# Performance work log

Measured on AMD Instinct MI355X. Metric: run time of the kernel, lower is better.

## Reference

```python
import jax, jax.numpy as jnp
import numpy as np

TEMPERATURE = 1.0
PRED_PER_IM = 100
INVALID = np.arange(60, 80)  # invalid class logit indices (constant)


def setup_inputs() -> dict:
    key = jax.random.key(0)
    k1, k2, k3, k4, k5 = jax.random.split(key, 5)
    B, Q, C = 256, 1000, 81
    return {
        "pred_logits": jax.random.normal(k1, (B, Q, C), jnp.float32),
        "pred_obj": jax.random.normal(k2, (B, Q), jnp.float32),
        "pred_boxes": jax.random.uniform(k3, (B, Q, 4), jnp.float32),  # cxcywh in [0,1)
        "pred_unk": jax.random.normal(k4, (B, Q), jnp.float32),
        "target_sizes": jax.random.uniform(k5, (B, 2), jnp.float32, minval=480.0, maxval=1333.0),  # (h, w)
    }


def _postprocess(pred_logits, pred_obj, pred_boxes, pred_unk, target_sizes):
    B, Q, C = pred_logits.shape
    # mask invalid classes with a huge negative logit
    logits = pred_logits.at[:, :, INVALID].set(-1e11)
    obj_prob = jnp.exp(-TEMPERATURE * pred_obj)[..., None]            # [B,Q,1]
    prob = obj_prob * jax.nn.sigmoid(logits)                          # [B,Q,C]
    prob = prob.at[:, :, INVALID].set(0.0)
    unk = jax.nn.sigmoid(pred_unk)                                    # [B,Q]
    prob = prob * (1.0 - unk[..., None])
    prob = prob.at[:, :, -1].set(obj_prob[..., 0] * unk)              # unknown class slot
    # flattened top-k over (query, class)
    scores, idx = jax.lax.top_k(prob.reshape(B, Q * C), PRED_PER_IM)  # [B,K]
    topk_boxes = idx // C
    labels = idx % C
    # cxcywh -> xyxy
    cx, cy, w, h = jnp.split(pred_boxes, 4, axis=-1)
    xyxy = jnp.concatenate([cx - 0.5 * w, cy - 0.5 * h, cx + 0.5 * w, cy + 0.5 * h], axis=-1)
    boxes = jnp.take_along_axis(xyxy, topk_boxes[..., None], axis=1)  # [B,K,4]
    img_h, img_w = target_sizes[:, 0], target_sizes[:, 1]
    scale = jnp.stack([img_w, img_h, img_w, img_h], axis=1)           # [B,4]
    boxes = boxes * scale[:, None, :]
    return scores, labels, boxes


def reference(pred_logits, pred_obj, pred_boxes, pred_unk, target_sizes):
    return _postprocess(pred_logits, pred_obj, pred_boxes, pred_unk, target_sizes)
```

## Files before the change

### kernel.cpp

```cpp
#include <hip/hip_runtime.h>
#include <math.h>

#define BATCH  256
#define NQ     1000
#define NC     81
#define QC     81000
#define CHUNKS (QC / 4)
#define TOPK   100
#define NBINS  4096
#define CAP    2048
#define NT     1024

__device__ __forceinline__ float sigmoidf(float x) {
    if (x >= 0.f) return 1.f / (1.f + expf(-x));
    float e = expf(x);
    return e / (1.f + e);
}

__device__ __forceinline__ float fast_sig(float x) {
    return __builtin_amdgcn_rcpf(1.f + __expf(-x));
}

struct Smem {
    float    P[NQ];
    float    Pm2[NQ];
    float    op[NQ];
    float    omun[NQ];
    float    last[NQ];
    unsigned hist[NBINS];
    uint2    cand[CAP];
    unsigned cnt;
    unsigned thr;
};

__device__ unsigned scan_threshold(Smem& s, int tid) {
    __syncthreads();
    if (tid < 64) {
        unsigned c = 0;
        #pragma unroll
        for (int j = 0; j < 64; j += 4) {
            uint4 h = *(const uint4*)&s.hist[tid * 64 + j];
            c += h.x + h.y + h.z + h.w;
        }
        unsigned ssum = c;
        #pragma unroll
        for (int off = 1; off < 64; off <<= 1) {
            unsigned o = __shfl_down(ssum, off, 64);
            if (tid + off < 64) ssum += o;
        }
        unsigned long long bal = __ballot(ssum >= TOPK);
        int cb = 63 - __clzll(bal);
        unsigned tb = 0;
        if (cb >= 0) {
            unsigned S_cb = __shfl(ssum, cb, 64);
            unsigned c_cb = __shfl(c, cb, 64);
            unsigned acc  = S_cb - c_cb;
            unsigned fs = s.hist[cb * 64 + tid];
            #pragma unroll
            for (int off = 1; off < 64; off <<= 1) {
                unsigned o = __shfl_down(fs, off, 64);
                if (tid + off < 64) fs += o;
            }
            unsigned long long bal2 = __ballot(acc + fs >= TOPK);
            int fb = 63 - __clzll(bal2);
            tb = (unsigned)(cb * 64 + fb);
        }
        if (tid == 0) s.thr = tb;
    }
    __syncthreads();
    return s.thr;
}

__device__ __forceinline__ void chunk_hist(Smem& s, const float4& v4, int q, int c,
                                           unsigned thbits) {
    float xs[4] = {v4.x, v4.y, v4.z, v4.w};
    #pragma unroll
    for (int k = 0; k < 4; ++k) {
        int ck = c + k, qk = q;
        if (ck >= NC) { ck -= NC; ++qk; }
        if (ck < 60) {
            unsigned u = __float_as_uint(s.P[qk] * fast_sig(xs[k]));
            if (u >= thbits) atomicAdd(&s.hist[u >> 19], 1u);
        }
    }
}

__device__ __forceinline__ void chunk_collect(Smem& s, const float4& v4, int q, int c,
                                              unsigned thbits) {
    float xs[4] = {v4.x, v4.y, v4.z, v4.w};
    #pragma unroll
    for (int k = 0; k < 4; ++k) {
        int ck = c + k, qk = q;
        if (ck >= NC) { ck -= NC; ++qk; }
        if (ck < 60) {
            unsigned u = __float_as_uint(s.P[qk] * fast_sig(xs[k]));
            if (u >= thbits) {
                float pv = (s.op[qk] * sigmoidf(xs[k])) * s.omun[qk];
                unsigned p = atomicAdd(&s.cnt, 1u);
                if (p < CAP)
                    s.cand[p] = make_uint2(__float_as_uint(pv), (unsigned)(qk * NC + ck));
            }
        }
    }
}

template <bool COLLECT>
__device__ void scan(Smem& s, const float4* __restrict__ lg4, unsigned thbits, int tid) {
    int q = (4 * tid) / NC;
    int c = 4 * tid - q * NC;
    for (int base = tid; base < CHUNKS; base += 4 * NT) {
        float4 vv[4]; bool dd[4]; int qs[4], cs[4];
        int qq = q, cc = c;
        #pragma unroll
        for (int t = 0; t < 4; ++t) {
            int i4 = base + t * NT;
            qs[t] = qq; cs[t] = cc;
            dd[t] = (i4 < CHUNKS) && (__float_as_uint(s.Pm2[qq]) >= thbits);
            if (dd[t]) vv[t] = lg4[i4];
            cc += 46; qq += 50; if (cc >= NC) { cc -= NC; ++qq; }
        }
        #pragma unroll
        for (int t = 0; t < 4; ++t) if (dd[t]) {
            if (COLLECT) chunk_collect(s, vv[t], qs[t], cs[t], thbits);
            else         chunk_hist   (s, vv[t], qs[t], cs[t], thbits);
        }
        c += 22; q += 202; if (c >= NC) { c -= NC; ++q; }
    }
}

__device__ void collect80(Smem& s, unsigned thbits, int tid) {
    for (int q = tid; q < NQ; q += NT) {
        unsigned u = __float_as_uint(s.last[q]);
        if (u >= thbits) {
            unsigned p = atomicAdd(&s.cnt, 1u);
            if (p < CAP) s.cand[p] = make_uint2(u, (unsigned)(q * NC + 80));
        }
    }
}

__global__ __launch_bounds__(NT) void postprocess_kernel(
    const float* __restrict__ logits,
    const float* __restrict__ obj,
    const float* __restrict__ boxes,
    const float* __restrict__ unk,
    const float* __restrict__ tsz,
    float* __restrict__ out)
{
    __shared__ Smem s;
    const int b   = blockIdx.x;
    const int tid = threadIdx.x;
    const float4* lg4 = (const float4*)(logits + (size_t)b * QC);

    {
        int i = tid * 4;
        *(uint4*)&s.hist[i] = make_uint4(0u, 0u, 0u, 0u);
    }
    if (tid == 0) s.cnt = 0;
    for (int q = tid; q < NQ; q += NT) {
        float op = expf(-obj[b * NQ + q]);
        float un = sigmoidf(unk[b * NQ + q]);
        float om = 1.f - un;
        s.op[q] = op; s.omun[q] = om; s.P[q] = op * om; s.last[q] = op * un;
    }
    __syncthreads();

    for (int q = tid; q < NQ; q += NT) {
        float pm = s.P[q];
        if (q + 1 < NQ) pm = fmaxf(pm, s.P[q + 1]);
        s.Pm2[q] = pm;
        atomicAdd(&s.hist[__float_as_uint(s.last[q]) >> 19], 1u);
    }

    unsigned t0 = scan_threshold(s, tid);

    scan<false>(s, lg4, t0 << 19, tid);

    unsigned tF = scan_threshold(s, tid);

    unsigned thC = ((tF >= 1) ? tF - 1 : 0) << 19;
    scan<true>(s, lg4, thC, tid);
    collect80(s, thC, tid);
    __syncthreads();

    if (s.cnt > CAP) {
        __syncthreads();
        if (tid == 0) s.cnt = 0;
        __syncthreads();
        scan<true>(s, lg4, tF << 19, tid);
        collect80(s, tF << 19, tid);
        __syncthreads();
    }

    const int m = (int)min(s.cnt, (unsigned)CAP);

    const float* bx = boxes + (size_t)b * NQ * 4;
    const float img_h = tsz[b * 2 + 0];
    const float img_w = tsz[b * 2 + 1];
    float* o_sc = out + (size_t)b * TOPK;
    float* o_lb = out + (size_t)BATCH * TOPK + (size_t)b * TOPK;
    float* o_bx = out + (size_t)2 * BATCH * TOPK + (size_t)b * TOPK * 4;

    for (int i = tid; i < m; i += NT) {
        uint2 ci = s.cand[i];
        int r = 0;
        for (int j = 0; j < m; ++j) {
            uint2 cj = s.cand[j];
            r += (cj.x > ci.x) || (cj.x == ci.x && cj.y < ci.y);
        }
        if (r < TOPK) {
            int ei = (int)ci.y;
            o_sc[r] = __uint_as_float(ci.x);
            o_lb[r] = (float)(ei % NC);
            int q = ei / NC;
            float cx = bx[q * 4 + 0];
            float cy = bx[q * 4 + 1];
            float w  = bx[q * 4 + 2];
            float h  = bx[q * 4 + 3];
            o_bx[r * 4 + 0] = (cx - 0.5f * w) * img_w;
            o_bx[r * 4 + 1] = (cy - 0.5f * h) * img_h;
            o_bx[r * 4 + 2] = (cx + 0.5f * w) * img_w;
            o_bx[r * 4 + 3] = (cy + 0.5f * h) * img_h;
        }
    }
}

extern "C" void kernel_launch(void* const* d_in, const int* in_sizes, int n_in,
                              void* d_out, int out_size, void* d_ws, size_t ws_size,
                              hipStream_t stream) {
    const float* pred_logits = (const float*)d_in[0];
    const float* pred_obj    = (const float*)d_in[1];
    const float* pred_boxes  = (const float*)d_in[2];
    const float* pred_unk    = (const float*)d_in[3];
    const float* target_sz   = (const float*)d_in[4];
    float* out = (float*)d_out;
    postprocess_kernel<<<BATCH, NT, 0, stream>>>(
        pred_logits, pred_obj, pred_boxes, pred_unk, target_sz, out);
}
```

Before: 145.3 us.

## Compact surviving query rows and scan only their logit chunks

Before each histogram or collect pass, a shared-memory list is built of the query rows whose max-probability bound reaches the threshold. Work is then spread evenly across only those rows' float4 chunks, instead of striding over every chunk and skipping dead ones by predicate. The intent is to remove idle loop iterations and load imbalance across threads when few rows survive. The cost is extra barriers, an atomic-based compaction step, and an integer divide by 21 per work item.

```diff
diff --git a/kernel.cpp b/kernel.cpp
--- a/kernel.cpp
+++ b/kernel.cpp
@@ -29,6 +29,8 @@
     float    last[NQ];
     unsigned hist[NBINS];
     uint2    cand[CAP];
+    int      rowlist[NQ];
+    unsigned nrows;
     unsigned cnt;
     unsigned thr;
 };
@@ -71,7 +73,8 @@
     return s.thr;
 }
 
-__device__ __forceinline__ void chunk_hist(Smem& s, const float4& v4, int q, int c,
+template <bool COLLECT>
+__device__ __forceinline__ void proc_chunk(Smem& s, const float4& v4, int q, int c,
                                            unsigned thbits) {
     float xs[4] = {v4.x, v4.y, v4.z, v4.w};
     #pragma unroll
@@ -80,51 +83,45 @@
         if (ck >= NC) { ck -= NC; ++qk; }
         if (ck < 60) {
             unsigned u = __float_as_uint(s.P[qk] * fast_sig(xs[k]));
-            if (u >= thbits) atomicAdd(&s.hist[u >> 19], 1u);
-        }
-    }
-}
-
-__device__ __forceinline__ void chunk_collect(Smem& s, const float4& v4, int q, int c,
-                                              unsigned thbits) {
-    float xs[4] = {v4.x, v4.y, v4.z, v4.w};
-    #pragma unroll
-    for (int k = 0; k < 4; ++k) {
-        int ck = c + k, qk = q;
-        if (ck >= NC) { ck -= NC; ++qk; }
-        if (ck < 60) {
-            unsigned u = __float_as_uint(s.P[qk] * fast_sig(xs[k]));
             if (u >= thbits) {
-                float pv = (s.op[qk] * sigmoidf(xs[k])) * s.omun[qk];
-                unsigned p = atomicAdd(&s.cnt, 1u);
-                if (p < CAP)
-                    s.cand[p] = make_uint2(__float_as_uint(pv), (unsigned)(qk * NC + ck));
+                if (!COLLECT) {
+                    atomicAdd(&s.hist[u >> 19], 1u);
+                } else {
+                    float pv = (s.op[qk] * sigmoidf(xs[k])) * s.omun[qk];
+                    unsigned p = atomicAdd(&s.cnt, 1u);
+                    if (p < CAP)
+                        s.cand[p] = make_uint2(__float_as_uint(pv),
+                                               (unsigned)(qk * NC + ck));
+                }
             }
         }
     }
 }
 
+__device__ void build_rows(Smem& s, unsigned thbits, int tid) {
+    __syncthreads();
+    if (tid == 0) s.nrows = 0;
+    __syncthreads();
+    for (int q = tid; q < NQ; q += NT)
+        if (__float_as_uint(s.Pm2[q]) >= thbits)
+            s.rowlist[atomicAdd(&s.nrows, 1u)] = q;
+    __syncthreads();
+}
+
 template <bool COLLECT>
-__device__ void scan(Smem& s, const float4* __restrict__ lg4, unsigned thbits, int tid) {
-    int q = (4 * tid) / NC;
-    int c = 4 * tid - q * NC;
-    for (int base = tid; base < CHUNKS; base += 4 * NT) {
-        float4 vv[4]; bool dd[4]; int qs[4], cs[4];
-        int qq = q, cc = c;
-        #pragma unroll
-        for (int t = 0; t < 4; ++t) {
-            int i4 = base + t * NT;
-            qs[t] = qq; cs[t] = cc;
-            dd[t] = (i4 < CHUNKS) && (__float_as_uint(s.Pm2[qq]) >= thbits);
-            if (dd[t]) vv[t] = lg4[i4];
-            cc += 46; qq += 50; if (cc >= NC) { cc -= NC; ++qq; }
-        }
-        #pragma unroll
-        for (int t = 0; t < 4; ++t) if (dd[t]) {
-            if (COLLECT) chunk_collect(s, vv[t], qs[t], cs[t], thbits);
-            else         chunk_hist   (s, vv[t], qs[t], cs[t], thbits);
-        }
-        c += 22; q += 202; if (c >= NC) { c -= NC; ++q; }
+__device__ void scan_rows(Smem& s, const float4* __restrict__ lg4,
+                          unsigned thbits, int tid) {
+    const int total = (int)s.nrows * 21;
+    for (int idx = tid; idx < total; idx += NT) {
+        int r  = idx / 21;
+        int j  = idx - r * 21;
+        int q  = s.rowlist[r];
+        int e0 = NC * q;
+        int i4 = ((e0 + 3) >> 2) + j;
+        if (4 * i4 < e0 + NC) {
+            float4 v4 = lg4[i4];
+            proc_chunk<COLLECT>(s, v4, q, 4 * i4 - e0, thbits);
+        }
     }
 }
 
@@ -151,10 +148,7 @@
     const int tid = threadIdx.x;
     const float4* lg4 = (const float4*)(logits + (size_t)b * QC);
 
-    {
-        int i = tid * 4;
-        *(uint4*)&s.hist[i] = make_uint4(0u, 0u, 0u, 0u);
-    }
+    *(uint4*)&s.hist[tid * 4] = make_uint4(0u, 0u, 0u, 0u);
     if (tid == 0) s.cnt = 0;
     for (int q = tid; q < NQ; q += NT) {
         float op = expf(-obj[b * NQ + q]);
@@ -173,12 +167,14 @@
 
     unsigned t0 = scan_threshold(s, tid);
 
-    scan<false>(s, lg4, t0 << 19, tid);
+    build_rows(s, t0 << 19, tid);
+    scan_rows<false>(s, lg4, t0 << 19, tid);
 
     unsigned tF = scan_threshold(s, tid);
 
     unsigned thC = ((tF >= 1) ? tF - 1 : 0) << 19;
-    scan<true>(s, lg4, thC, tid);
+    build_rows(s, thC, tid);
+    scan_rows<true>(s, lg4, thC, tid);
     collect80(s, thC, tid);
     __syncthreads();
 
@@ -186,7 +182,7 @@
         __syncthreads();
         if (tid == 0) s.cnt = 0;
         __syncthreads();
-        scan<true>(s, lg4, tF << 19, tid);
+        scan_rows<true>(s, lg4, tF << 19, tid);
         collect80(s, tF << 19, tid);
         __syncthreads();
     }
```

Measured after the change: 136.8 us. 1.06x faster.
